# Performance work log

Hardware: AMD Instinct MI355X
Metric: run time of the kernel (lower is better)

Reference implementation:

```python
import jax, jax.numpy as jnp
import numpy as np

K = 25          # moving-average kernel_size
P = 24          # periodicity
PAD_LEN = 5     # median padding window (padding_mode='median')


def setup_inputs() -> dict:
    key = jax.random.key(0)
    x = jax.random.normal(key, (64, 128, 8192), dtype=jnp.float32)
    return {"x": x}


def _decompose(x):
    B, C, L = x.shape
    half = (K - 1) // 2  # 12

    # --- moving_average_decomposition with 'median' padding ---
    # torch.median over an odd window (5) == jnp.median
    front = jnp.median(x[:, :, :PAD_LEN], axis=2, keepdims=True)   # [B,C,1]
    end = jnp.median(x[:, :, -PAD_LEN:], axis=2, keepdims=True)    # [B,C,1]
    xp = jnp.concatenate(
        [jnp.repeat(front, half, axis=2), x, jnp.repeat(end, half, axis=2)],
        axis=2,
    )  # [B,C,L+K-1]

    # AvgPool1d(kernel=K, stride=1) via prefix-sum difference (single pass)
    cs = jnp.cumsum(xp, axis=-1)
    cs = jnp.concatenate([jnp.zeros_like(cs[:, :, :1]), cs], axis=-1)
    trend = (cs[:, :, K:] - cs[:, :, :-K]) / K                      # [B,C,L]
    res = x - trend

    # --- per-phase seasonal mean (vectorized replacement of python loop) ---
    pad_len = L % P
    if pad_len > 0:
        # original: cat(res, res[:, :, -P:-pad_len]) -> length divisible by P
        xpad = jnp.concatenate([res, res[:, :, -P:-pad_len]], axis=-1)
    else:
        xpad = res
    n = xpad.shape[-1] // P
    # mean over occurrences of each phase i (== mean of x_padded[:, :, i::P])
    seasonal = jnp.mean(xpad.reshape(B, C, n, P), axis=2)           # [B,C,P]
    out_seasonal = jnp.tile(seasonal, (1, 1, n))[:, :, :L]          # broadcast back
    out_residual = res - out_seasonal
    return out_residual, trend, out_seasonal


def reference(x):
    return _decompose(x)
```

## Files before the change

kernel.cpp:

```cpp
#include <hip/hip_runtime.h>
#include <cstdint>

namespace {
constexpr int LROW   = 8192;
constexpr int KWIN   = 25;
constexpr int HALF   = (KWIN - 1) / 2;
constexpr int PERIOD = 24;
constexpr int NOCC   = 342;
constexpr int NTHR   = 256;
constexpr int GRP    = LROW / (4 * NTHR);
constexpr int RPB    = 16;
}

__device__ __forceinline__ void ce(float& x, float& y) {
    float lo = fminf(x, y), hi = fmaxf(x, y);
    x = lo; y = hi;
}

__device__ __forceinline__ float median5(float a, float b, float c, float d, float e) {
    ce(a, b); ce(d, e); ce(c, e); ce(c, d); ce(a, d); ce(a, c);
    ce(b, e); ce(b, d); ce(b, c);
    return c;
}

__device__ __forceinline__ void stage_row(const float* __restrict__ xr,
                                          float* ldsbuf, int t) {
    #pragma unroll
    for (int j = 0; j < GRP; ++j) {
        int g = 4 * (t + NTHR * j);
        __builtin_amdgcn_global_load_lds(
            (const __attribute__((address_space(1))) uint32_t*)(xr + g),
            (__attribute__((address_space(3))) uint32_t*)(ldsbuf + g),
            16, 0, 0);
    }
}

__global__ __launch_bounds__(NTHR, 2) void decomp_kernel(
    const float* __restrict__ x,
    float* __restrict__ out_res,
    float* __restrict__ out_trend,
    float* __restrict__ out_seas)
{
    __shared__ __align__(16) float buf[2][LROW];
    __shared__ float part[240];
    __shared__ float seasonal[PERIOD];

    const int t = threadIdx.x;
    const int b = blockIdx.x;
    const int rstride = gridDim.x;

    auto row_base = [&](int i) -> size_t {
        return ((size_t)(b + i * rstride)) * (size_t)LROW;
    };

    stage_row(x + row_base(0), buf[0], t);
    stage_row(x + row_base(1), buf[1], t);
    __syncthreads();

    for (int i = 0; i < RPB; ++i) {
        const int cur = i & 1;
        const size_t base = row_base(i);
        float* xs = buf[cur];

        float resv[GRP][4];
        #pragma unroll
        for (int j = 0; j < GRP; ++j) {
            int g = 4 * (t + NTHR * j);
            float v[28];
            if (g >= HALF && g <= LROW - 16) {
                #pragma unroll
                for (int q = 0; q < 7; ++q) {
                    float4 f = *reinterpret_cast<const float4*>(xs + g - HALF + 4 * q);
                    v[4*q+0] = f.x; v[4*q+1] = f.y; v[4*q+2] = f.z; v[4*q+3] = f.w;
                }
            } else {
                float med = (g < HALF)
                    ? median5(xs[0], xs[1], xs[2], xs[3], xs[4])
                    : median5(xs[LROW-5], xs[LROW-4], xs[LROW-3], xs[LROW-2], xs[LROW-1]);
                #pragma unroll
                for (int q = 0; q < 28; ++q) {
                    int idx = g - HALF + q;
                    v[q] = (idx < 0 || idx >= LROW) ? med : xs[idx];
                }
            }
            float s = 0.f;
            #pragma unroll
            for (int q = 0; q < KWIN; ++q) s += v[q];
            constexpr float inv = 1.0f / (float)KWIN;
            float w1 = s  - v[0] + v[25];
            float w2 = w1 - v[1] + v[26];
            float w3 = w2 - v[2] + v[27];
            float t0 = s * inv, t1 = w1 * inv, t2 = w2 * inv, t3 = w3 * inv;
            resv[j][0] = v[12] - t0;
            resv[j][1] = v[13] - t1;
            resv[j][2] = v[14] - t2;
            resv[j][3] = v[15] - t3;
            *reinterpret_cast<float4*>(out_trend + base + g) =
                make_float4(t0, t1, t2, t3);
        }
        __syncthreads();

        #pragma unroll
        for (int j = 0; j < GRP; ++j) {
            int g = 4 * (t + NTHR * j);
            *reinterpret_cast<float4*>(xs + g) =
                make_float4(resv[j][0], resv[j][1], resv[j][2], resv[j][3]);
        }
        __syncthreads();

        if (t < 240) {
            const int p = t / 10, s0 = t % 10;
            float acc = 0.f;
            for (int k = s0; k < NOCC; k += 10) {
                int m = PERIOD * k + p;
                if (m >= LROW) m -= PERIOD;
                acc += xs[m];
            }
            part[t] = acc;
        }
        __syncthreads();

        if (i + 2 < RPB) stage_row(x + row_base(i + 2), buf[cur], t);

        if (t < PERIOD) {
            float s = 0.f;
            #pragma unroll
            for (int q = 0; q < 10; ++q) s += part[t * 10 + q];
            seasonal[t] = s / (float)NOCC;
        }
        __syncthreads();

        #pragma unroll
        for (int j = 0; j < GRP; ++j) {
            int g = 4 * (t + NTHR * j);
            int ph = g % PERIOD;
            float s0 = seasonal[ph + 0];
            float s1 = seasonal[ph + 1];
            float s2 = seasonal[ph + 2];
            float s3 = seasonal[ph + 3];
            *reinterpret_cast<float4*>(out_seas + base + g) =
                make_float4(s0, s1, s2, s3);
            *reinterpret_cast<float4*>(out_res + base + g) =
                make_float4(resv[j][0] - s0, resv[j][1] - s1,
                            resv[j][2] - s2, resv[j][3] - s3);
        }
    }
}

extern "C" void kernel_launch(void* const* d_in, const int* in_sizes, int n_in,
                              void* d_out, int out_size, void* d_ws, size_t ws_size,
                              hipStream_t stream) {
    const float* x = (const float*)d_in[0];
    float* out = (float*)d_out;
    const size_t n = (size_t)in_sizes[0];
    const int rows = (int)(n / (size_t)LROW);
    const int nblk = rows / RPB;
    decomp_kernel<<<nblk, NTHR, 0, stream>>>(x, out, out + n, out + 2 * n);
}
```

Baseline: 226.4 us.

## Replace persistent double-buffered row loop with one block per row

Drops the persistent design where each block handled 16 rows with double-buffered async LDS staging. Now each block processes a single row with a single LDS buffer, launching one block per row at up to 4 blocks per CU. Trend stores are deferred to the final phase alongside the seasonal and residual stores. The intent is to rely on occupancy rather than explicit prefetch to hide latency. In exchange it loses the load/compute overlap and adds launch overhead for 8192 blocks, and holding the trend values in registers raises register pressure.

Result: slower. 415.4 us (+83.5%).

```diff
diff --git a/kernel.cpp b/kernel.cpp
--- a/kernel.cpp
+++ b/kernel.cpp
@@ -9,7 +9,6 @@
 constexpr int NOCC   = 342;
 constexpr int NTHR   = 256;
 constexpr int GRP    = LROW / (4 * NTHR);
-constexpr int RPB    = 16;
 }
 
 __device__ __forceinline__ void ce(float& x, float& y) {
@@ -23,127 +22,111 @@
     return c;
 }
 
-__device__ __forceinline__ void stage_row(const float* __restrict__ xr,
-                                          float* ldsbuf, int t) {
+__global__ __launch_bounds__(NTHR, 4) void decomp_kernel(
+    const float* __restrict__ x,
+    float* __restrict__ out_res,
+    float* __restrict__ out_trend,
+    float* __restrict__ out_seas)
+{
+    __shared__ __align__(16) float xs[LROW];
+    __shared__ float part[240];
+    __shared__ float seasonal[PERIOD];
+
+    const int t = threadIdx.x;
+    const size_t base = (size_t)blockIdx.x * LROW;
+    const float* xr = x + base;
+
     #pragma unroll
     for (int j = 0; j < GRP; ++j) {
         int g = 4 * (t + NTHR * j);
         __builtin_amdgcn_global_load_lds(
             (const __attribute__((address_space(1))) uint32_t*)(xr + g),
-            (__attribute__((address_space(3))) uint32_t*)(ldsbuf + g),
+            (__attribute__((address_space(3))) uint32_t*)(xs + g),
             16, 0, 0);
     }
-}
-
-__global__ __launch_bounds__(NTHR, 2) void decomp_kernel(
-    const float* __restrict__ x,
-    float* __restrict__ out_res,
-    float* __restrict__ out_trend,
-    float* __restrict__ out_seas)
-{
-    __shared__ __align__(16) float buf[2][LROW];
-    __shared__ float part[240];
-    __shared__ float seasonal[PERIOD];
-
-    const int t = threadIdx.x;
-    const int b = blockIdx.x;
-    const int rstride = gridDim.x;
-
-    auto row_base = [&](int i) -> size_t {
-        return ((size_t)(b + i * rstride)) * (size_t)LROW;
-    };
-
-    stage_row(x + row_base(0), buf[0], t);
-    stage_row(x + row_base(1), buf[1], t);
     __syncthreads();
 
-    for (int i = 0; i < RPB; ++i) {
-        const int cur = i & 1;
-        const size_t base = row_base(i);
-        float* xs = buf[cur];
+    float resv[GRP][4], trendv[GRP][4];
+    #pragma unroll
+    for (int j = 0; j < GRP; ++j) {
+        int g = 4 * (t + NTHR * j);
+        float v[28];
+        if (g >= HALF && g <= LROW - 16) {
+            #pragma unroll
+            for (int q = 0; q < 7; ++q) {
+                float4 f = *reinterpret_cast<const float4*>(xs + g - HALF + 4 * q);
+                v[4*q+0] = f.x; v[4*q+1] = f.y; v[4*q+2] = f.z; v[4*q+3] = f.w;
+            }
+        } else {
+            float med = (g < HALF)
+                ? median5(xs[0], xs[1], xs[2], xs[3], xs[4])
+                : median5(xs[LROW-5], xs[LROW-4], xs[LROW-3], xs[LROW-2], xs[LROW-1]);
+            #pragma unroll
+            for (int q = 0; q < 28; ++q) {
+                int idx = g - HALF + q;
+                v[q] = (idx < 0 || idx >= LROW) ? med : xs[idx];
+            }
+        }
+        float s = 0.f;
+        #pragma unroll
+        for (int q = 0; q < KWIN; ++q) s += v[q];
+        constexpr float inv = 1.0f / (float)KWIN;
+        float w1 = s  - v[0] + v[25];
+        float w2 = w1 - v[1] + v[26];
+        float w3 = w2 - v[2] + v[27];
+        trendv[j][0] = s  * inv;
+        trendv[j][1] = w1 * inv;
+        trendv[j][2] = w2 * inv;
+        trendv[j][3] = w3 * inv;
+        resv[j][0] = v[12] - trendv[j][0];
+        resv[j][1] = v[13] - trendv[j][1];
+        resv[j][2] = v[14] - trendv[j][2];
+        resv[j][3] = v[15] - trendv[j][3];
+    }
+    __syncthreads();
 
-        float resv[GRP][4];
+    #pragma unroll
+    for (int j = 0; j < GRP; ++j) {
+        int g = 4 * (t + NTHR * j);
+        *reinterpret_cast<float4*>(xs + g) =
+            make_float4(resv[j][0], resv[j][1], resv[j][2], resv[j][3]);
+    }
+    __syncthreads();
+
+    if (t < 240) {
+        const int p = t / 10, s0 = t % 10;
+        float acc = 0.f;
+        for (int k = s0; k < NOCC; k += 10) {
+            int m = PERIOD * k + p;
+            if (m >= LROW) m -= PERIOD;
+            acc += xs[m];
+        }
+        part[t] = acc;
+    }
+    __syncthreads();
+    if (t < PERIOD) {
+        float s = 0.f;
         #pragma unroll
-        for (int j = 0; j < GRP; ++j) {
-            int g = 4 * (t + NTHR * j);
-            float v[28];
-            if (g >= HALF && g <= LROW - 16) {
-                #pragma unroll
-                for (int q = 0; q < 7; ++q) {
-                    float4 f = *reinterpret_cast<const float4*>(xs + g - HALF + 4 * q);
-                    v[4*q+0] = f.x; v[4*q+1] = f.y; v[4*q+2] = f.z; v[4*q+3] = f.w;
-                }
-            } else {
-                float med = (g < HALF)
-                    ? median5(xs[0], xs[1], xs[2], xs[3], xs[4])
-                    : median5(xs[LROW-5], xs[LROW-4], xs[LROW-3], xs[LROW-2], xs[LROW-1]);
-                #pragma unroll
-                for (int q = 0; q < 28; ++q) {
-                    int idx = g - HALF + q;
-                    v[q] = (idx < 0 || idx >= LROW) ? med : xs[idx];
-                }
-            }
-            float s = 0.f;
-            #pragma unroll
-            for (int q = 0; q < KWIN; ++q) s += v[q];
-            constexpr float inv = 1.0f / (float)KWIN;
-            float w1 = s  - v[0] + v[25];
-            float w2 = w1 - v[1] + v[26];
-            float w3 = w2 - v[2] + v[27];
-            float t0 = s * inv, t1 = w1 * inv, t2 = w2 * inv, t3 = w3 * inv;
-            resv[j][0] = v[12] - t0;
-            resv[j][1] = v[13] - t1;
-            resv[j][2] = v[14] - t2;
-            resv[j][3] = v[15] - t3;
-            *reinterpret_cast<float4*>(out_trend + base + g) =
-                make_float4(t0, t1, t2, t3);
-        }
-        __syncthreads();
+        for (int q = 0; q < 10; ++q) s += part[t * 10 + q];
+        seasonal[t] = s / (float)NOCC;
+    }
+    __syncthreads();
 
-        #pragma unroll
-        for (int j = 0; j < GRP; ++j) {
-            int g = 4 * (t + NTHR * j);
-            *reinterpret_cast<float4*>(xs + g) =
-                make_float4(resv[j][0], resv[j][1], resv[j][2], resv[j][3]);
-        }
-        __syncthreads();
-
-        if (t < 240) {
-            const int p = t / 10, s0 = t % 10;
-            float acc = 0.f;
-            for (int k = s0; k < NOCC; k += 10) {
-                int m = PERIOD * k + p;
-                if (m >= LROW) m -= PERIOD;
-                acc += xs[m];
-            }
-            part[t] = acc;
-        }
-        __syncthreads();
-
-        if (i + 2 < RPB) stage_row(x + row_base(i + 2), buf[cur], t);
-
-        if (t < PERIOD) {
-            float s = 0.f;
-            #pragma unroll
-            for (int q = 0; q < 10; ++q) s += part[t * 10 + q];
-            seasonal[t] = s / (float)NOCC;
-        }
-        __syncthreads();
-
-        #pragma unroll
-        for (int j = 0; j < GRP; ++j) {
-            int g = 4 * (t + NTHR * j);
-            int ph = g % PERIOD;
-            float s0 = seasonal[ph + 0];
-            float s1 = seasonal[ph + 1];
-            float s2 = seasonal[ph + 2];
-            float s3 = seasonal[ph + 3];
-            *reinterpret_cast<float4*>(out_seas + base + g) =
-                make_float4(s0, s1, s2, s3);
-            *reinterpret_cast<float4*>(out_res + base + g) =
-                make_float4(resv[j][0] - s0, resv[j][1] - s1,
-                            resv[j][2] - s2, resv[j][3] - s3);
-        }
+    #pragma unroll
+    for (int j = 0; j < GRP; ++j) {
+        int g = 4 * (t + NTHR * j);
+        int ph = g % PERIOD;
+        float s0 = seasonal[ph + 0];
+        float s1 = seasonal[ph + 1];
+        float s2 = seasonal[ph + 2];
+        float s3 = seasonal[ph + 3];
+        *reinterpret_cast<float4*>(out_trend + base + g) =
+            make_float4(trendv[j][0], trendv[j][1], trendv[j][2], trendv[j][3]);
+        *reinterpret_cast<float4*>(out_seas + base + g) =
+            make_float4(s0, s1, s2, s3);
+        *reinterpret_cast<float4*>(out_res + base + g) =
+            make_float4(resv[j][0] - s0, resv[j][1] - s1,
+                        resv[j][2] - s2, resv[j][3] - s3);
     }
 }
 
@@ -154,6 +137,5 @@
     float* out = (float*)d_out;
     const size_t n = (size_t)in_sizes[0];
     const int rows = (int)(n / (size_t)LROW);
-    const int nblk = rows / RPB;
-    decomp_kernel<<<nblk, NTHR, 0, stream>>>(x, out, out + n, out + 2 * n);
+    decomp_kernel<<<rows, NTHR, 0, stream>>>(x, out, out + n, out + 2 * n);
 }
```
